# Kernel optimization log

Hardware: AMD Instinct MI355X
Metric: run time of the kernel (lower is better)

## Reference

```python
import jax, jax.numpy as jnp
import numpy as np

N_NODES = 100000
N_EDGES = 1600000
IN_CH, CH1, CH2 = 256, 256, 128


def gcn_conv(x, W, b, src, dst, ew, n):
    """PyG GCNConv: h = x @ W; out[i] = sum_j norm_ij * h[j] + b, with self-loops
    (weight 1.0) and symmetric normalization D^-1/2 A D^-1/2."""
    loop = jnp.arange(n)
    src_f = jnp.concatenate([src, loop])
    dst_f = jnp.concatenate([dst, loop])
    ew_f = jnp.concatenate([ew, jnp.ones((n,), dtype=x.dtype)])
    deg = jax.ops.segment_sum(ew_f, dst_f, num_segments=n)  # weighted in-degree incl self-loop
    dinv = jnp.where(deg > 0, jax.lax.rsqrt(deg), 0.0)
    norm = dinv[src_f] * ew_f * dinv[dst_f]                  # [E+N]
    h = x @ W                                                # [N, C_out]
    msg = h[src_f] * norm[:, None]                           # gather + scale, [E+N, C_out]
    out = jax.ops.segment_sum(msg, dst_f, num_segments=n)   # scatter-add to targets
    return out + b


def setup_inputs() -> dict:
    key = jax.random.key(0)
    ks = jax.random.split(key, 7)
    x = jax.random.normal(ks[0], (N_NODES, IN_CH), dtype=jnp.float32)
    edge_index = jax.random.randint(ks[1], (2, N_EDGES), 0, N_NODES, dtype=jnp.int64)
    edge_weight = jax.random.uniform(ks[2], (N_EDGES,), dtype=jnp.float32)
    # Glorot-style init for GCN weights, zero bias (PyG defaults)
    W1 = jax.random.normal(ks[3], (IN_CH, CH1), dtype=jnp.float32) * (1.0 / np.sqrt(IN_CH))
    b1 = jnp.zeros((CH1,), dtype=jnp.float32)
    W2 = jax.random.normal(ks[4], (CH1, CH2), dtype=jnp.float32) * (1.0 / np.sqrt(CH1))
    b2 = jnp.zeros((CH2,), dtype=jnp.float32)
    return {"x": x, "edge_index": edge_index, "edge_weight": edge_weight,
            "W1": W1, "b1": b1, "W2": W2, "b2": b2}


def reference(x, edge_index, edge_weight, W1, b1, W2, b2):
    src, dst = edge_index[0], edge_index[1]
    n = x.shape[0]
    x1 = gcn_conv(x, W1, b1, src, dst, edge_weight, n)
    x1 = jax.nn.gelu(x1, approximate=False)  # torch F.gelu default is exact erf
    # dropout is identity in eval mode (deterministic reference)
    x2 = gcn_conv(x1, W2, b2, src, dst, edge_weight, n)
    return x2
```

## Files before the change

kernel.cpp:

```cpp
#include <hip/hip_runtime.h>
#include <math.h>


#define CH1 256
#define CH2 128
#define MAXDEG 64

using bf16x8 = __attribute__((ext_vector_type(8))) short;
using f32x4  = __attribute__((ext_vector_type(4))) float;

__device__ __forceinline__ ushort f2bf(float f) {
    unsigned u = __float_as_uint(f);
    u = u + 0x7fffu + ((u >> 16) & 1u);
    return (ushort)(u >> 16);
}
__device__ __forceinline__ float bf_lo(unsigned u) {
    return __uint_as_float(u << 16);
}
__device__ __forceinline__ float bf_hi(unsigned u) {
    return __uint_as_float(u & 0xffff0000u);
}
__device__ __forceinline__ float dinv_from(unsigned long long a) {
    return rsqrtf(1.0f + (float)(a & 0xFFFFFFFFFFull) * (1.0f / 16777216.0f));
}

__global__ void zero_acc(unsigned long long* acc, int n) {
    int i = blockIdx.x * blockDim.x + threadIdx.x;
    if (i < n) acc[i] = 0ull;
}

__global__ __launch_bounds__(256) void fused_count_cvt_w(
    const int* __restrict__ ei, const float* __restrict__ ew,
    unsigned long long* __restrict__ acc, unsigned* __restrict__ pairs,
    int E, int EB,
    const float* __restrict__ x, ushort* __restrict__ xb, int n8, int CB,
    const float* __restrict__ W1, ushort* __restrict__ W1T, int w1n, int W1B,
    const float* __restrict__ W2, ushort* __restrict__ W2T, int w2n) {
    int bid = blockIdx.x;
    if (bid < EB) {
        int base = bid * 256 + threadIdx.x;
        int stride = EB * 256;
        int e[8]; int s[8]; int d[8]; float w[8];
#pragma unroll
        for (int k = 0; k < 8; ++k) e[k] = base + k * stride;
#pragma unroll
        for (int k = 0; k < 8; ++k)
            if (e[k] < E) {
                s[k] = ei[e[k]];
                d[k] = ei[E + e[k]];
                w[k] = ew[e[k]];
            }
        unsigned long long old[8];
#pragma unroll
        for (int k = 0; k < 8; ++k)
            if (e[k] < E) {
                unsigned fx = (unsigned)__float2uint_rn(w[k] * 16777216.0f);
                old[k] = atomicAdd(&acc[d[k]],
                                   (1ull << 40) | (unsigned long long)fx);
            }
#pragma unroll
        for (int k = 0; k < 8; ++k)
            if (e[k] < E) {
                int r = (int)(old[k] >> 40);
                if (r < MAXDEG) {
                    unsigned cb = (unsigned)(f2bf(w[k]) & 0x7FFF);
                    pairs[(size_t)d[k] * MAXDEG + r] =
                        (cb << 17) | (unsigned)s[k];
                }
            }
    } else if (bid < EB + CB) {
        int i = (bid - EB) * 256 + threadIdx.x;
        if (i < n8) {
            float4 a = reinterpret_cast<const float4*>(x)[i * 2];
            float4 b = reinterpret_cast<const float4*>(x)[i * 2 + 1];
            uint4 o;
            o.x = (unsigned)f2bf(a.x) | ((unsigned)f2bf(a.y) << 16);
            o.y = (unsigned)f2bf(a.z) | ((unsigned)f2bf(a.w) << 16);
            o.z = (unsigned)f2bf(b.x) | ((unsigned)f2bf(b.y) << 16);
            o.w = (unsigned)f2bf(b.z) | ((unsigned)f2bf(b.w) << 16);
            reinterpret_cast<uint4*>(xb)[i] = o;
        }
    } else if (bid < EB + CB + W1B) {
        int idx = (bid - EB - CB) * 256 + threadIdx.x;
        if (idx < w1n) {
            int k = idx / CH1, nn = idx % CH1;
            W1T[nn * CH1 + k] = f2bf(W1[idx]);
        }
    } else {
        int idx = (bid - EB - CB - W1B) * 256 + threadIdx.x;
        if (idx < w2n) {
            int k = idx / CH2, nn = idx % CH2;
            W2T[nn * CH1 + k] = f2bf(W2[idx]);
        }
    }
}

template <int SCALE>
__global__ __launch_bounds__(256) void gemm_bf16(
    const ushort* __restrict__ A, const ushort* __restrict__ BT,
    ushort* __restrict__ C, const unsigned long long* __restrict__ acc64,
    int M, int N, int K) {
    __shared__ __align__(16) ushort Als[128 * 32];
    __shared__ __align__(16) ushort Bls[128 * 32];

    const int t = threadIdx.x;
    const int w = t >> 6;
    const int lane = t & 63;
    const int wr = w >> 1, wc = w & 1;
    const int row0 = blockIdx.x * 128;
    const int col0 = blockIdx.y * 128;

    f32x4 acc[4][4] = {};

    for (int k0 = 0; k0 < K; k0 += 32) {
#pragma unroll
        for (int i = 0; i < 2; ++i) {
            int c = (w * 2 + i) * 64 + lane;
            int row = c >> 2;
            int kg = c & 3;
            int arow = row0 + row; if (arow > M - 1) arow = M - 1;
            const ushort* gA = A + (size_t)arow * K + k0 + kg * 8;
            const ushort* gB = BT + (size_t)(col0 + row) * K + k0 + kg * 8;
            __builtin_amdgcn_global_load_lds(
                (const __attribute__((address_space(1))) unsigned*)gA,
                (__attribute__((address_space(3))) unsigned*)&Als[(size_t)(w * 2 + i) * 512],
                16, 0, 0);
            __builtin_amdgcn_global_load_lds(
                (const __attribute__((address_space(1))) unsigned*)gB,
                (__attribute__((address_space(3))) unsigned*)&Bls[(size_t)(w * 2 + i) * 512],
                16, 0, 0);
        }
        __syncthreads();

        bf16x8 afr[4], bfr[4];
#pragma unroll
        for (int m = 0; m < 4; ++m)
            afr[m] = *reinterpret_cast<const bf16x8*>(
                &Als[(wr * 64 + m * 16 + (lane & 15)) * 32 + (lane >> 4) * 8]);
#pragma unroll
        for (int nn = 0; nn < 4; ++nn)
            bfr[nn] = *reinterpret_cast<const bf16x8*>(
                &Bls[(wc * 64 + nn * 16 + (lane & 15)) * 32 + (lane >> 4) * 8]);
#pragma unroll
        for (int m = 0; m < 4; ++m)
#pragma unroll
            for (int nn = 0; nn < 4; ++nn)
                acc[m][nn] = __builtin_amdgcn_mfma_f32_16x16x32_bf16(
                    afr[m], bfr[nn], acc[m][nn], 0, 0, 0);
        __syncthreads();
    }

#pragma unroll
    for (int m = 0; m < 4; ++m) {
#pragma unroll
        for (int j = 0; j < 4; ++j) {
            int row = row0 + wr * 64 + m * 16 + (lane >> 4) * 4 + j;
            if (row < M) {
                float sc = 1.0f;
                if constexpr (SCALE) sc = dinv_from(acc64[row]);
#pragma unroll
                for (int nn = 0; nn < 4; ++nn) {
                    int col = col0 + wc * 64 + nn * 16 + (lane & 15);
                    C[(size_t)row * N + col] = f2bf(acc[m][nn][j] * sc);
                }
            }
        }
    }
}

__device__ __forceinline__ float gelu_exact(float x) {
    return 0.5f * x * (1.0f + erff(x * 0.70710678118654752f));
}

template <int C, int APPLY_GELU, int SCALE_OUT, int OUT_BF16>
__global__ __launch_bounds__(256) void aggregate6(
    const ushort* __restrict__ h, const unsigned long long* __restrict__ acc64,
    const unsigned* __restrict__ pairs, const float* __restrict__ bias,
    void* __restrict__ outv, int n) {
    constexpr int LPE = C / 8;
    constexpr int EPG = 64 / LPE;
    int wid = threadIdx.x >> 6;
    int lane = threadIdx.x & 63;
    int g = lane / LPE;
    int l = lane % LPE;
    int node = blockIdx.x * 4 + wid;
    if (node >= n) return;

    unsigned long long a = acc64[node];
    int deg = min((int)(a >> 40), MAXDEG);
    float di = dinv_from(a);

    const unsigned* pb = pairs + (size_t)node * MAXDEG;
    const ushort* hl = h + l * 8;

    float acc[8];
#pragma unroll
    for (int c = 0; c < 8; ++c) acc[c] = 0.f;

    for (int t = 0; t < deg; t += 4 * EPG) {
        unsigned pk[4];
        float cf[4];
        uint4 gv[4];
#pragma unroll
        for (int k = 0; k < 4; ++k) {
            int idx = t + k * EPG + g;
            int cl = min(idx, deg - 1);
            pk[k] = pb[cl];
            cf[k] = (idx < deg) ? __uint_as_float((pk[k] >> 17) << 16) : 0.f;
        }
#pragma unroll
        for (int k = 0; k < 4; ++k)
            gv[k] = *reinterpret_cast<const uint4*>(
                hl + (size_t)(pk[k] & 0x1FFFFu) * C);
#pragma unroll
        for (int k = 0; k < 4; ++k) {
            acc[0] += cf[k] * bf_lo(gv[k].x);
            acc[1] += cf[k] * bf_hi(gv[k].x);
            acc[2] += cf[k] * bf_lo(gv[k].y);
            acc[3] += cf[k] * bf_hi(gv[k].y);
            acc[4] += cf[k] * bf_lo(gv[k].z);
            acc[5] += cf[k] * bf_hi(gv[k].z);
            acc[6] += cf[k] * bf_lo(gv[k].w);
            acc[7] += cf[k] * bf_hi(gv[k].w);
        }
    }

#pragma unroll
    for (int off = LPE; off < 64; off <<= 1) {
#pragma unroll
        for (int c = 0; c < 8; ++c) acc[c] += __shfl_xor(acc[c], off);
    }

    uint4 sv = *reinterpret_cast<const uint4*>(hl + (size_t)node * C);
    float self[8] = {bf_lo(sv.x), bf_hi(sv.x), bf_lo(sv.y), bf_hi(sv.y),
                     bf_lo(sv.z), bf_hi(sv.z), bf_lo(sv.w), bf_hi(sv.w)};
    float4 bv0 = *reinterpret_cast<const float4*>(bias + l * 8);
    float4 bv1 = *reinterpret_cast<const float4*>(bias + l * 8 + 4);
    float bb[8] = {bv0.x, bv0.y, bv0.z, bv0.w, bv1.x, bv1.y, bv1.z, bv1.w};

    float res[8];
#pragma unroll
    for (int c = 0; c < 8; ++c) {
        float v = di * (acc[c] + self[c]) + bb[c];
        if (APPLY_GELU) v = gelu_exact(v);
        if (SCALE_OUT) v = v * di;
        res[c] = v;
    }

    if (g == 0) {
        if constexpr (OUT_BF16) {
            uint4 o;
            o.x = (unsigned)f2bf(res[0]) | ((unsigned)f2bf(res[1]) << 16);
            o.y = (unsigned)f2bf(res[2]) | ((unsigned)f2bf(res[3]) << 16);
            o.z = (unsigned)f2bf(res[4]) | ((unsigned)f2bf(res[5]) << 16);
            o.w = (unsigned)f2bf(res[6]) | ((unsigned)f2bf(res[7]) << 16);
            *reinterpret_cast<uint4*>((ushort*)outv + (size_t)node * C + l * 8) = o;
        } else {
            float* op = (float*)outv + (size_t)node * C + l * 8;
            float4 o0 = {res[0], res[1], res[2], res[3]};
            float4 o1 = {res[4], res[5], res[6], res[7]};
            *reinterpret_cast<float4*>(op) = o0;
            *reinterpret_cast<float4*>(op + 4) = o1;
        }
    }
}

extern "C" void kernel_launch(void* const* d_in, const int* in_sizes, int n_in,
                              void* d_out, int out_size, void* d_ws, size_t ws_size,
                              hipStream_t stream) {
    const float* x  = (const float*)d_in[0];
    const int*   ei = (const int*)d_in[1];
    const float* ew = (const float*)d_in[2];
    const float* W1 = (const float*)d_in[3];
    const float* b1 = (const float*)d_in[4];
    const float* W2 = (const float*)d_in[5];
    const float* b2 = (const float*)d_in[6];
    float* out = (float*)d_out;

    int n = in_sizes[0] / CH1;
    int E = in_sizes[1] / 2;

    char* ws = (char*)d_ws;
    size_t off = 0;
    auto alloc = [&](size_t bytes) -> void* {
        void* p = ws + off;
        off += (bytes + 255) & ~(size_t)255;
        return p;
    };
    unsigned long long* acc64 = (unsigned long long*)alloc((size_t)n * 8);
    unsigned* pairs  = (unsigned*)alloc((size_t)n * MAXDEG * 4);
    ushort* xb       = (ushort*)alloc((size_t)n * CH1 * 2);
    ushort* h        = (ushort*)alloc((size_t)n * CH1 * 2);
    ushort* x1b      = (ushort*)alloc((size_t)n * CH1 * 2);
    ushort* W1T      = (ushort*)alloc((size_t)CH1 * CH1 * 2);
    ushort* W2T      = (ushort*)alloc((size_t)CH2 * CH1 * 2);

    int gn = (n + 255) / 256;

    int EB = (E + 2047) / 2048;
    int n8 = n * CH1 / 8;
    int CB = (n8 + 255) / 256;
    int w1n = CH1 * CH1, W1B = (w1n + 255) / 256;
    int w2n = CH1 * CH2, W2B = (w2n + 255) / 256;
    zero_acc<<<gn, 256, 0, stream>>>(acc64, n);
    fused_count_cvt_w<<<EB + CB + W1B + W2B, 256, 0, stream>>>(
        ei, ew, acc64, pairs, E, EB, x, xb, n8, CB,
        W1, W1T, w1n, W1B, W2, W2T, w2n);

    int gx = (n + 127) / 128;
    int ngb = (n + 3) / 4;

    dim3 g1(gx, CH1 / 128);
    gemm_bf16<1><<<g1, 256, 0, stream>>>(xb, W1T, h, acc64, n, CH1, CH1);
    aggregate6<CH1, 1, 1, 1><<<ngb, 256, 0, stream>>>(h, acc64, pairs, b1, x1b, n);

    dim3 g2(gx, CH2 / 128);
    gemm_bf16<0><<<g2, 256, 0, stream>>>(x1b, W2T, h, acc64, n, CH2, CH1);
    aggregate6<CH2, 0, 0, 0><<<ngb, 256, 0, stream>>>(h, acc64, pairs, b2, out, n);
}
```

Measured before the change: 369.9 us.

## Fuse edge counting with layer-1 GEMM reading fp32 x directly

The layer-1 GEMM now converts fp32 x to bf16 on the fly into LDS and shares a launch with the edge-count/CSR-fill blocks, removing the separate x-to-bf16 conversion pass and its intermediate buffer. Because the GEMM can no longer depend on finished degrees, the source-side dinv scaling moves out of the GEMM epilogue into the aggregation, where each edge coefficient is multiplied by a gathered dinv[src] from a new dinv array. A small dinv kernel is added, and zeroing plus weight transposes are merged into one prep kernel. The cost is an extra per-edge 4-byte gather in layer-1 aggregation and one more kernel launch.

```diff
diff --git a/kernel.cpp b/kernel.cpp
--- a/kernel.cpp
+++ b/kernel.cpp
@@ -24,18 +24,38 @@
     return rsqrtf(1.0f + (float)(a & 0xFFFFFFFFFFull) * (1.0f / 16777216.0f));
 }
 
-__global__ void zero_acc(unsigned long long* acc, int n) {
-    int i = blockIdx.x * blockDim.x + threadIdx.x;
-    if (i < n) acc[i] = 0ull;
-}
-
-__global__ __launch_bounds__(256) void fused_count_cvt_w(
+__global__ __launch_bounds__(256) void prep_kernel(
+    unsigned long long* __restrict__ acc, int n, int gn,
+    const float* __restrict__ W1, ushort* __restrict__ W1T, int w1n, int W1B,
+    const float* __restrict__ W2, ushort* __restrict__ W2T, int w2n) {
+    int bid = blockIdx.x;
+    if (bid < gn) {
+        int i = bid * 256 + threadIdx.x;
+        if (i < n) acc[i] = 0ull;
+    } else if (bid < gn + W1B) {
+        int idx = (bid - gn) * 256 + threadIdx.x;
+        if (idx < w1n) {
+            int k = idx / CH1, nn = idx % CH1;
+            W1T[nn * CH1 + k] = f2bf(W1[idx]);
+        }
+    } else {
+        int idx = (bid - gn - W1B) * 256 + threadIdx.x;
+        if (idx < w2n) {
+            int k = idx / CH2, nn = idx % CH2;
+            W2T[nn * CH1 + k] = f2bf(W2[idx]);
+        }
+    }
+}
+
+__global__ __launch_bounds__(256) void count_gemm1(
     const int* __restrict__ ei, const float* __restrict__ ew,
     unsigned long long* __restrict__ acc, unsigned* __restrict__ pairs,
     int E, int EB,
-    const float* __restrict__ x, ushort* __restrict__ xb, int n8, int CB,
-    const float* __restrict__ W1, ushort* __restrict__ W1T, int w1n, int W1B,
-    const float* __restrict__ W2, ushort* __restrict__ W2T, int w2n) {
+    const float* __restrict__ x, const ushort* __restrict__ W1T,
+    ushort* __restrict__ h, int M, int gx) {
+    __shared__ __align__(16) ushort Als[128 * 32];
+    __shared__ __align__(16) ushort Bls[128 * 32];
+
     int bid = blockIdx.x;
     if (bid < EB) {
         int base = bid * 256 + threadIdx.x;
@@ -68,38 +88,96 @@
                         (cb << 17) | (unsigned)s[k];
                 }
             }
-    } else if (bid < EB + CB) {
-        int i = (bid - EB) * 256 + threadIdx.x;
-        if (i < n8) {
-            float4 a = reinterpret_cast<const float4*>(x)[i * 2];
-            float4 b = reinterpret_cast<const float4*>(x)[i * 2 + 1];
-            uint4 o;
-            o.x = (unsigned)f2bf(a.x) | ((unsigned)f2bf(a.y) << 16);
-            o.y = (unsigned)f2bf(a.z) | ((unsigned)f2bf(a.w) << 16);
-            o.z = (unsigned)f2bf(b.x) | ((unsigned)f2bf(b.y) << 16);
-            o.w = (unsigned)f2bf(b.z) | ((unsigned)f2bf(b.w) << 16);
-            reinterpret_cast<uint4*>(xb)[i] = o;
-        }
-    } else if (bid < EB + CB + W1B) {
-        int idx = (bid - EB - CB) * 256 + threadIdx.x;
-        if (idx < w1n) {
-            int k = idx / CH1, nn = idx % CH1;
-            W1T[nn * CH1 + k] = f2bf(W1[idx]);
-        }
-    } else {
-        int idx = (bid - EB - CB - W1B) * 256 + threadIdx.x;
-        if (idx < w2n) {
-            int k = idx / CH2, nn = idx % CH2;
-            W2T[nn * CH1 + k] = f2bf(W2[idx]);
-        }
-    }
-}
-
-template <int SCALE>
+        return;
+    }
+
+    int g = bid - EB;
+    int bx = g % gx, by = g / gx;
+    const int t = threadIdx.x;
+    const int w = t >> 6;
+    const int lane = t & 63;
+    const int wr = w >> 1, wc = w & 1;
+    const int row0 = bx * 128;
+    const int col0 = by * 128;
+    const int K = CH1, N = CH1;
+
+    f32x4 acc4[4][4] = {};
+
+    const int ar = t >> 1;
+    const int half = t & 1;
+
+    for (int k0 = 0; k0 < K; k0 += 32) {
+#pragma unroll
+        for (int i = 0; i < 2; ++i) {
+            int c = (w * 2 + i) * 64 + lane;
+            int row = c >> 2;
+            int kg = c & 3;
+            const ushort* gB = W1T + (size_t)(col0 + row) * K + k0 + kg * 8;
+            __builtin_amdgcn_global_load_lds(
+                (const __attribute__((address_space(1))) unsigned*)gB,
+                (__attribute__((address_space(3))) unsigned*)&Bls[(size_t)(w * 2 + i) * 512],
+                16, 0, 0);
+        }
+        int arow = row0 + ar; if (arow > M - 1) arow = M - 1;
+        const float4* gA = reinterpret_cast<const float4*>(
+            x + (size_t)arow * K + k0 + half * 16);
+        float4 f0 = gA[0], f1 = gA[1], f2 = gA[2], f3 = gA[3];
+        uint4 p0, p1;
+        p0.x = (unsigned)f2bf(f0.x) | ((unsigned)f2bf(f0.y) << 16);
+        p0.y = (unsigned)f2bf(f0.z) | ((unsigned)f2bf(f0.w) << 16);
+        p0.z = (unsigned)f2bf(f1.x) | ((unsigned)f2bf(f1.y) << 16);
+        p0.w = (unsigned)f2bf(f1.z) | ((unsigned)f2bf(f1.w) << 16);
+        p1.x = (unsigned)f2bf(f2.x) | ((unsigned)f2bf(f2.y) << 16);
+        p1.y = (unsigned)f2bf(f2.z) | ((unsigned)f2bf(f2.w) << 16);
+        p1.z = (unsigned)f2bf(f3.x) | ((unsigned)f2bf(f3.y) << 16);
+        p1.w = (unsigned)f2bf(f3.z) | ((unsigned)f2bf(f3.w) << 16);
+        uint4* dstA = reinterpret_cast<uint4*>(&Als[ar * 32 + half * 16]);
+        dstA[0] = p0;
+        dstA[1] = p1;
+        __syncthreads();
+
+        bf16x8 afr[4], bfr[4];
+#pragma unroll
+        for (int m = 0; m < 4; ++m)
+            afr[m] = *reinterpret_cast<const bf16x8*>(
+                &Als[(wr * 64 + m * 16 + (lane & 15)) * 32 + (lane >> 4) * 8]);
+#pragma unroll
+        for (int nn = 0; nn < 4; ++nn)
+            bfr[nn] = *reinterpret_cast<const bf16x8*>(
+                &Bls[(wc * 64 + nn * 16 + (lane & 15)) * 32 + (lane >> 4) * 8]);
+#pragma unroll
+        for (int m = 0; m < 4; ++m)
+#pragma unroll
+            for (int nn = 0; nn < 4; ++nn)
+                acc4[m][nn] = __builtin_amdgcn_mfma_f32_16x16x32_bf16(
+                    afr[m], bfr[nn], acc4[m][nn], 0, 0, 0);
+        __syncthreads();
+    }
+
+#pragma unroll
+    for (int m = 0; m < 4; ++m) {
+#pragma unroll
+        for (int nn = 0; nn < 4; ++nn) {
+            f32x4 v = acc4[m][nn];
+            int col = col0 + wc * 64 + nn * 16 + (lane & 15);
+#pragma unroll
+            for (int j = 0; j < 4; ++j) {
+                int row = row0 + wr * 64 + m * 16 + (lane >> 4) * 4 + j;
+                if (row < M) h[(size_t)row * N + col] = f2bf(v[j]);
+            }
+        }
+    }
+}
+
+__global__ void dinv_kernel(const unsigned long long* __restrict__ acc,
+                            float* __restrict__ dinv, int n) {
+    int i = blockIdx.x * blockDim.x + threadIdx.x;
+    if (i < n) dinv[i] = dinv_from(acc[i]);
+}
+
 __global__ __launch_bounds__(256) void gemm_bf16(
     const ushort* __restrict__ A, const ushort* __restrict__ BT,
-    ushort* __restrict__ C, const unsigned long long* __restrict__ acc64,
-    int M, int N, int K) {
+    ushort* __restrict__ C, int M, int N, int K) {
     __shared__ __align__(16) ushort Als[128 * 32];
     __shared__ __align__(16) ushort Bls[128 * 32];
 
@@ -153,16 +231,13 @@
 #pragma unroll
     for (int m = 0; m < 4; ++m) {
 #pragma unroll
-        for (int j = 0; j < 4; ++j) {
-            int row = row0 + wr * 64 + m * 16 + (lane >> 4) * 4 + j;
-            if (row < M) {
-                float sc = 1.0f;
-                if constexpr (SCALE) sc = dinv_from(acc64[row]);
-#pragma unroll
-                for (int nn = 0; nn < 4; ++nn) {
-                    int col = col0 + wc * 64 + nn * 16 + (lane & 15);
-                    C[(size_t)row * N + col] = f2bf(acc[m][nn][j] * sc);
-                }
+        for (int nn = 0; nn < 4; ++nn) {
+            f32x4 v = acc[m][nn];
+            int col = col0 + wc * 64 + nn * 16 + (lane & 15);
+#pragma unroll
+            for (int j = 0; j < 4; ++j) {
+                int row = row0 + wr * 64 + m * 16 + (lane >> 4) * 4 + j;
+                if (row < M) C[(size_t)row * N + col] = f2bf(v[j]);
             }
         }
     }
@@ -172,11 +247,11 @@
     return 0.5f * x * (1.0f + erff(x * 0.70710678118654752f));
 }
 
-template <int C, int APPLY_GELU, int SCALE_OUT, int OUT_BF16>
-__global__ __launch_bounds__(256) void aggregate6(
+template <int C, int APPLY_GELU, int SCALE_OUT, int OUT_BF16, int GDINV>
+__global__ __launch_bounds__(256) void aggregate7(
     const ushort* __restrict__ h, const unsigned long long* __restrict__ acc64,
-    const unsigned* __restrict__ pairs, const float* __restrict__ bias,
-    void* __restrict__ outv, int n) {
+    const unsigned* __restrict__ pairs, const float* __restrict__ dinv,
+    const float* __restrict__ bias, void* __restrict__ outv, int n) {
     constexpr int LPE = C / 8;
     constexpr int EPG = 64 / LPE;
     int wid = threadIdx.x >> 6;
@@ -206,7 +281,9 @@
             int idx = t + k * EPG + g;
             int cl = min(idx, deg - 1);
             pk[k] = pb[cl];
-            cf[k] = (idx < deg) ? __uint_as_float((pk[k] >> 17) << 16) : 0.f;
+            float c0 = __uint_as_float((pk[k] >> 17) << 16);
+            if constexpr (GDINV) c0 *= dinv[pk[k] & 0x1FFFFu];
+            cf[k] = (idx < deg) ? c0 : 0.f;
         }
 #pragma unroll
         for (int k = 0; k < 4; ++k)
@@ -238,10 +315,13 @@
     float4 bv1 = *reinterpret_cast<const float4*>(bias + l * 8 + 4);
     float bb[8] = {bv0.x, bv0.y, bv0.z, bv0.w, bv1.x, bv1.y, bv1.z, bv1.w};
 
+    float di2 = di * di;
     float res[8];
 #pragma unroll
     for (int c = 0; c < 8; ++c) {
-        float v = di * (acc[c] + self[c]) + bb[c];
+        float v;
+        if constexpr (GDINV) v = di * acc[c] + di2 * self[c] + bb[c];
+        else                 v = di * (acc[c] + self[c]) + bb[c];
         if (APPLY_GELU) v = gelu_exact(v);
         if (SCALE_OUT) v = v * di;
         res[c] = v;
@@ -289,32 +369,36 @@
     };
     unsigned long long* acc64 = (unsigned long long*)alloc((size_t)n * 8);
     unsigned* pairs  = (unsigned*)alloc((size_t)n * MAXDEG * 4);
-    ushort* xb       = (ushort*)alloc((size_t)n * CH1 * 2);
+    float*  dinv     = (float*)alloc((size_t)n * 4);
     ushort* h        = (ushort*)alloc((size_t)n * CH1 * 2);
     ushort* x1b      = (ushort*)alloc((size_t)n * CH1 * 2);
     ushort* W1T      = (ushort*)alloc((size_t)CH1 * CH1 * 2);
     ushort* W2T      = (ushort*)alloc((size_t)CH2 * CH1 * 2);
 
     int gn = (n + 255) / 256;
-
-    int EB = (E + 2047) / 2048;
-    int n8 = n * CH1 / 8;
-    int CB = (n8 + 255) / 256;
     int w1n = CH1 * CH1, W1B = (w1n + 255) / 256;
     int w2n = CH1 * CH2, W2B = (w2n + 255) / 256;
-    zero_acc<<<gn, 256, 0, stream>>>(acc64, n);
-    fused_count_cvt_w<<<EB + CB + W1B + W2B, 256, 0, stream>>>(
-        ei, ew, acc64, pairs, E, EB, x, xb, n8, CB,
-        W1, W1T, w1n, W1B, W2, W2T, w2n);
-
+
+    prep_kernel<<<gn + W1B + W2B, 256, 0, stream>>>(acc64, n, gn,
+                                                    W1, W1T, w1n, W1B,
+                                                    W2, W2T, w2n);
+
+    int EB = (E + 2047) / 2048;
     int gx = (n + 127) / 128;
+    int G1B = gx * (CH1 / 128);
+    count_gemm1<<<EB + G1B, 256, 0, stream>>>(ei, ew, acc64, pairs, E, EB,
+                                              x, W1T, h, n, gx);
+
+    dinv_kernel<<<gn, 256, 0, stream>>>(acc64, dinv, n);
+
     int ngb = (n + 3) / 4;
 
-    dim3 g1(gx, CH1 / 128);
-    gemm_bf16<1><<<g1, 256, 0, stream>>>(xb, W1T, h, acc64, n, CH1, CH1);
-    aggregate6<CH1, 1, 1, 1><<<ngb, 256, 0, stream>>>(h, acc64, pairs, b1, x1b, n);
+    aggregate7<CH1, 1, 1, 1, 1><<<ngb, 256, 0, stream>>>(h, acc64, pairs, dinv,
+                                                         b1, x1b, n);
 
     dim3 g2(gx, CH2 / 128);
-    gemm_bf16<0><<<g2, 256, 0, stream>>>(x1b, W2T, h, acc64, n, CH2, CH1);
-    aggregate6<CH2, 0, 0, 0><<<ngb, 256, 0, stream>>>(h, acc64, pairs, b2, out, n);
-}
+    gemm_bf16<<<g2, 256, 0, stream>>>(x1b, W2T, h, n, CH2, CH1);
+
+    aggregate7<CH2, 0, 0, 0, 0><<<ngb, 256, 0, stream>>>(h, acc64, pairs, dinv,
+                                                         b2, out, n);
+}
```

Measured after the change: 356.8 us (median of 2 runs). 1.04x faster.
